# Kernel optimization log

Hardware: AMD Instinct MI355X
Metric: run time of the kernel (lower is better)

Reference implementation:

```python
import jax, jax.numpy as jnp
import numpy as np

# Dimensions (match init_kwargs / input_specs)
N, F, E = 50000, 256, 200000   # nodes, in-features, edges
H, C = 4, 128                  # heads, per-head channels (hidden_dim)
G, NC = 256, 10                # graphs in batch, num_classes
EPS = 1e-16                    # PyG softmax denominator epsilon


def _lin(key, fin, fout):
    kw, kb = jax.random.split(key)
    W = jax.random.normal(kw, (fin, fout), jnp.float32) / np.float32(np.sqrt(fin))
    b = jax.random.normal(kb, (fout,), jnp.float32) * 0.01
    return W, b


def setup_inputs() -> dict:
    key = jax.random.key(0)
    ks = jax.random.split(key, 16)
    x = jax.random.normal(ks[0], (N, F), jnp.float32)
    edge_index = jax.random.randint(ks[1], (2, E), 0, N)
    batch = jnp.sort(jax.random.randint(ks[2], (N,), 0, G))
    d = {"x": x, "edge_index": edge_index, "batch": batch}
    # layer1: in=F, out=H*C (concat=True); layer2: in=H*C, out=C (concat=False, skip -> C)
    d["Wq1"], d["bq1"] = _lin(ks[3], F, H * C)
    d["Wk1"], d["bk1"] = _lin(ks[4], F, H * C)
    d["Wv1"], d["bv1"] = _lin(ks[5], F, H * C)
    d["Ws1"], d["bs1"] = _lin(ks[6], F, H * C)
    d["Wq2"], d["bq2"] = _lin(ks[7], H * C, H * C)
    d["Wk2"], d["bk2"] = _lin(ks[8], H * C, H * C)
    d["Wv2"], d["bv2"] = _lin(ks[9], H * C, H * C)
    d["Ws2"], d["bs2"] = _lin(ks[10], H * C, C)
    d["Wfc"], d["bfc"] = _lin(ks[11], C, NC)
    return d


def _tconv(x, src, dst, Wq, bq, Wk, bk, Wv, bv, Ws, bs, concat):
    """PyG TransformerConv (root_weight=True, beta=False), eval mode (no dropout)."""
    n = x.shape[0]
    q = (x @ Wq + bq).reshape(n, H, C)
    k = (x @ Wk + bk).reshape(n, H, C)
    v = (x @ Wv + bv).reshape(n, H, C)
    # per-edge scores: query from dst node i, key/value from src node j
    alpha = jnp.einsum('ehc,ehc->eh', q[dst], k[src]) / jnp.float32(np.sqrt(C))  # [E,H]
    m = jax.ops.segment_max(alpha, dst, num_segments=n)          # [N,H]
    e = jnp.exp(alpha - m[dst])                                  # [E,H]
    s = jax.ops.segment_sum(e, dst, num_segments=n)              # [N,H]
    a = e / (s[dst] + EPS)                                       # segment softmax over dst
    msg = jax.ops.segment_sum(a[:, :, None] * v[src], dst, num_segments=n)  # [N,H,C]
    out = msg.reshape(n, H * C) if concat else msg.mean(axis=1)
    return out + x @ Ws + bs  # root/skip connection


def reference(x, edge_index, batch,
              Wq1, bq1, Wk1, bk1, Wv1, bv1, Ws1, bs1,
              Wq2, bq2, Wk2, bk2, Wv2, bv2, Ws2, bs2,
              Wfc, bfc):
    src, dst = edge_index[0], edge_index[1]
    h = jax.nn.elu(_tconv(x, src, dst, Wq1, bq1, Wk1, bk1, Wv1, bv1, Ws1, bs1, True))
    # dropout is identity in eval mode
    h = jax.nn.elu(_tconv(h, src, dst, Wq2, bq2, Wk2, bk2, Wv2, bv2, Ws2, bs2, False))
    cnt = jax.ops.segment_sum(jnp.ones((h.shape[0],), h.dtype), batch, num_segments=G)
    pooled = jax.ops.segment_sum(h, batch, num_segments=G) / jnp.maximum(cnt, 1.0)[:, None]
    return jax.nn.log_softmax(pooled @ Wfc + bfc, axis=1)  # [G, NC]
```

## Files before the change

kernel.cpp:

```cpp
#include <hip/hip_runtime.h>
#include <math.h>
#include <stdint.h>

#define N_NODES 50000
#define FEAT    256
#define EDGES   200000
#define HEADS   4
#define CH      128
#define HID     512
#define NGRAPH  256
#define NCLS    10

typedef unsigned short ushort_t;
typedef unsigned int uint_t;
typedef __attribute__((ext_vector_type(8))) short bf16x8;
typedef __attribute__((ext_vector_type(4))) float f32x4;
typedef __attribute__((ext_vector_type(2))) float f32x2;

__device__ __forceinline__ ushort_t f2bf(float f) {
  uint_t u = __float_as_uint(f);
  u += 0x7FFF + ((u >> 16) & 1);
  return (ushort_t)(u >> 16);
}
__device__ __forceinline__ float bf2f(ushort_t h) {
  return __uint_as_float(((uint_t)h) << 16);
}
__device__ __forceinline__ float elu1(float x) {
  return x > 0.f ? x : __expf(x) - 1.f;
}
__device__ __forceinline__ float fastrcp(float x) {
  return __builtin_amdgcn_rcpf(x);
}
__device__ __forceinline__ void unpack8(uint4 w, float* f) {
  f[0] = bf2f((ushort_t)w.x); f[1] = bf2f((ushort_t)(w.x >> 16));
  f[2] = bf2f((ushort_t)w.y); f[3] = bf2f((ushort_t)(w.y >> 16));
  f[4] = bf2f((ushort_t)w.z); f[5] = bf2f((ushort_t)(w.z >> 16));
  f[6] = bf2f((ushort_t)w.w); f[7] = bf2f((ushort_t)(w.w >> 16));
}
__device__ __forceinline__ void unpack8_fp8(uint2 w, float* f) {
  f32x2 a = __builtin_amdgcn_cvt_pk_f32_fp8((int)w.x, false);
  f32x2 b = __builtin_amdgcn_cvt_pk_f32_fp8((int)w.x, true);
  f32x2 c = __builtin_amdgcn_cvt_pk_f32_fp8((int)w.y, false);
  f32x2 d = __builtin_amdgcn_cvt_pk_f32_fp8((int)w.y, true);
  f[0] = a[0]; f[1] = a[1]; f[2] = b[0]; f[3] = b[1];
  f[4] = c[0]; f[5] = c[1]; f[6] = d[0]; f[7] = d[1];
}
__device__ __forceinline__ uint_t pack4_fp8(float f0, float f1, float f2, float f3) {
  int v = __builtin_amdgcn_cvt_pk_fp8_f32(f0, f1, 0, false);
  v = __builtin_amdgcn_cvt_pk_fp8_f32(f2, f3, v, true);
  return (uint_t)v;
}


__global__ __launch_bounds__(256) void gemm_bt(
    const ushort_t* __restrict__ A, const ushort_t* __restrict__ Bt,
    const float* __restrict__ bias, char* __restrict__ Cb,
    char* __restrict__ Cb2, int M, int K, int nct, int mode) {
  __shared__ __align__(16) ushort_t smem[24576];
  const int tid = threadIdx.x;
  const int lane = tid & 63, wave = tid >> 6;
  const int wr = wave >> 1, wc = wave & 1;

  int b = blockIdx.x;
  int per = nct << 3;
  int grp = b / per;
  int rem = b - grp * per;
  int rloc = rem & 7;
  int ct = rem >> 3;
  const int rowBase = (grp * 8 + rloc) * 128;
  const int colBase = ct * 128;
  if (rowBase >= M) return;

  const int s0 = tid, s1 = tid + 256;
  const int rl0 = s0 >> 2, cg0 = (s0 & 3) ^ ((rl0 >> 1) & 3);
  const int rl1 = s1 >> 2, cg1 = (s1 & 3) ^ ((rl1 >> 1) & 3);
  int ra0 = rowBase + rl0; ra0 = ra0 < M ? ra0 : M - 1;
  int ra1 = rowBase + rl1; ra1 = ra1 < M ? ra1 : M - 1;
  const ushort_t* pa0 = A + (size_t)ra0 * K + cg0 * 8;
  const ushort_t* pa1 = A + (size_t)ra1 * K + cg1 * 8;
  const ushort_t* pb0 = Bt + (size_t)(colBase + rl0) * K + cg0 * 8;
  const ushort_t* pb1 = Bt + (size_t)(colBase + rl1) * K + cg1 * 8;
  const int dA0 = s0 * 8, dA1 = s1 * 8;
  const int dB0 = 4096 + s0 * 8, dB1 = 4096 + s1 * 8;

#define GLL(gp, loff)  __builtin_amdgcn_global_load_lds( \
      (const __attribute__((address_space(1))) uint_t*)(gp), \
      (__attribute__((address_space(3))) uint_t*)(smem + (loff)), 16, 0, 0)

  const int nt = K >> 5;
  GLL(pa0, dA0);            GLL(pa1, dA1);
  GLL(pb0, dB0);            GLL(pb1, dB1);
  GLL(pa0 + 32, 8192 + dA0); GLL(pa1 + 32, 8192 + dA1);
  GLL(pb0 + 32, 8192 + dB0); GLL(pb1 + 32, 8192 + dB1);
  pa0 += 64; pa1 += 64; pb0 += 64; pb1 += 64;

  const int fr = lane & 15, c0 = lane >> 4;
  const int pswz = (c0 ^ ((fr >> 1) & 3)) * 8;
  const int aOff = (wr * 64 + fr) * 32 + pswz;
  const int bOff = 4096 + (wc * 64 + fr) * 32 + pswz;

  f32x4 acc[4][4] = {};
  asm volatile("s_waitcnt vmcnt(4)" ::: "memory");
  __builtin_amdgcn_s_barrier();
  __builtin_amdgcn_sched_barrier(0);

  int cur = 0, nxt = 2;
  for (int t = 0; t < nt; ++t) {
    const ushort_t* bufc = smem + cur * 8192;
    const bool pf = (t + 2) < nt;
    bf16x8 af[4], bfr[4];
    af[0] = *(const bf16x8*)(bufc + aOff);
#pragma unroll
    for (int j = 0; j < 4; ++j) bfr[j] = *(const bf16x8*)(bufc + bOff + j * 512);
#pragma unroll
    for (int i = 1; i < 4; ++i) af[i] = *(const bf16x8*)(bufc + aOff + i * 512);
    if (pf) {
      int lo = nxt * 8192;
      GLL(pa0, lo + dA0); GLL(pa1, lo + dA1);
      GLL(pb0, lo + dB0); GLL(pb1, lo + dB1);
      pa0 += 32; pa1 += 32; pb0 += 32; pb1 += 32;
    }
#pragma unroll
    for (int i = 0; i < 4; ++i)
#pragma unroll
      for (int j = 0; j < 4; ++j)
        acc[i][j] = __builtin_amdgcn_mfma_f32_16x16x32_bf16(af[i], bfr[j], acc[i][j], 0, 0, 0);
    asm volatile("s_waitcnt lgkmcnt(0)" ::: "memory");
    if (pf)                asm volatile("s_waitcnt vmcnt(4)" ::: "memory");
    else if (t + 1 < nt)   asm volatile("s_waitcnt vmcnt(0)" ::: "memory");
    __builtin_amdgcn_s_barrier();
    __builtin_amdgcn_sched_barrier(0);
    cur = cur == 2 ? 0 : cur + 1;
    nxt = nxt == 2 ? 0 : nxt + 1;
  }
#undef GLL

  char* obase; int ostride, koff, isfp8;
  if (mode == 1) {
    int H = colBase >> 9, sel = (colBase >> 7) & 3;
    if (sel == 0)      { obase = Cb;  ostride = 2304; koff = H * 256; isfp8 = 0; }
    else if (sel == 3) { obase = Cb2; ostride = 1024; koff = H * 256; isfp8 = 0; }
    else { obase = Cb; ostride = 2304;
           koff = 1024 + H * 256 + (sel == 2 ? 8 : 0); isfp8 = 1; }
  } else {
    obase = Cb; ostride = 2304;
    if (colBase == 768) { koff = 2048; isfp8 = 0; }
    else {
      int n2 = (colBase < 768) ? colBase : colBase - 896;
      int hb = (colBase < 768) ? 0 : 2;
      int hh = hb + n2 / 384, r = n2 % 384, sel = r >> 7;
      if (sel == 0) { koff = hh * 256; isfp8 = 0; }
      else          { koff = 1024 + hh * 256 + (sel == 2 ? 8 : 0); isfp8 = 1; }
    }
  }

  ushort_t* wbuf = smem + wave * 2048;
  const int rq = lane >> 4, fc = lane & 15;
  float bv[4];
#pragma unroll
  for (int j = 0; j < 4; ++j) bv[j] = bias[colBase + wc * 64 + j * 16 + fc];
#pragma unroll
  for (int h = 0; h < 2; ++h) {
#pragma unroll
    for (int ii = 0; ii < 2; ++ii) {
      int i = h * 2 + ii;
#pragma unroll
      for (int j = 0; j < 4; ++j)
#pragma unroll
        for (int r = 0; r < 4; ++r) {
          int rl = ii * 16 + rq * 4 + r;
          int cl = j * 16 + fc;
          int cs = cl ^ (rq << 4);
          wbuf[rl * 64 + cs] = f2bf(acc[i][j][r] + bv[j]);
        }
    }
    int ci = lane & 7;
    int rbase = lane >> 3;
#pragma unroll
    for (int rg = 0; rg < 4; ++rg) {
      int rr = rg * 8 + rbase;
      int rowg = rowBase + wr * 64 + h * 32 + rr;
      int cg = ci ^ (((rr >> 2) & 3) << 1);
      uint4 val = *(const uint4*)(wbuf + rr * 64 + (ci << 3));
      if (rowg < M) {
        char* dstRow = obase + (size_t)rowg * ostride + koff;
        if (!isfp8) {
          *(uint4*)(dstRow + (wc * 64 + cg * 8) * 2) = val;
        } else {
          float f[8];
          f[0] = bf2f((ushort_t)val.x); f[1] = bf2f((ushort_t)(val.x >> 16));
          f[2] = bf2f((ushort_t)val.y); f[3] = bf2f((ushort_t)(val.y >> 16));
          f[4] = bf2f((ushort_t)val.z); f[5] = bf2f((ushort_t)(val.z >> 16));
          f[6] = bf2f((ushort_t)val.w); f[7] = bf2f((ushort_t)(val.w >> 16));
          uint2 o;
          o.x = pack4_fp8(f[0], f[1], f[2], f[3]);
          o.y = pack4_fp8(f[4], f[5], f[6], f[7]);
          *(uint2*)(dstRow + ((wc * 8 + cg) << 4)) = o;
        }
      }
    }
  }
}

#define L1_W   (2048 * FEAT)
#define L2_W   (1664 * HID)
#define T1     512
#define T2     832
#define NB_CVT  12500
#define NB_TP   (T1 + T2)
#define NB_BIAS 15
#define NB_ZERO 196

__global__ __launch_bounds__(256) void prep_all(
    const float* __restrict__ x, ushort_t* __restrict__ xb,
    const float* __restrict__ Wq1, const float* __restrict__ Wk1,
    const float* __restrict__ Wv1, const float* __restrict__ Ws1,
    const float* __restrict__ Wq2, const float* __restrict__ Wk2,
    const float* __restrict__ Wv2, const float* __restrict__ Ws2,
    const float* __restrict__ bq1, const float* __restrict__ bk1,
    const float* __restrict__ bv1, const float* __restrict__ bs1,
    const float* __restrict__ bq2, const float* __restrict__ bk2,
    const float* __restrict__ bv2, const float* __restrict__ bs2,
    ushort_t* __restrict__ W1t, ushort_t* __restrict__ W2t,
    float* __restrict__ Bh1, float* __restrict__ Bh2,
    int* __restrict__ deg, int* __restrict__ counter,
    int* __restrict__ gstart, int* __restrict__ gend) {
  __shared__ float tile[32][33];
  int blk = blockIdx.x;
  if (blk < NB_CVT) {
    int i = blk * 256 + threadIdx.x;
    float4 f = *(const float4*)(x + (size_t)i * 4);
    uint_t lo = (uint_t)f2bf(f.x) | ((uint_t)f2bf(f.y) << 16);
    uint_t hi = (uint_t)f2bf(f.z) | ((uint_t)f2bf(f.w) << 16);
    ((uint2*)xb)[i] = make_uint2(lo, hi);
    return;
  }
  blk -= NB_CVT;
  if (blk < NB_TP) {
    int t = blk;
    const float* W; int ldw, c0, n0, k0, ldk; ushort_t* dst;
    if (t < T1) {
      int nb = t >> 3, kb = t & 7;
      n0 = nb * 32; k0 = kb * 32; ldk = FEAT; dst = W1t;
      int p = n0 >> 10, n1 = n0 & 1023, hh = n1 >> 9, sel = (n1 >> 7) & 3;
      c0 = (2 * p + hh) * CH + (n1 & (CH - 1));
      W = sel == 0 ? Wq1 : sel == 1 ? Wk1 : sel == 2 ? Wv1 : Ws1;
      ldw = HID;
    } else {
      t -= T1;
      int nb = t >> 4, kb = t & 15;
      n0 = nb * 32; k0 = kb * 32; ldk = HID; dst = W2t;
      if (n0 < 768 || n0 >= 896) {
        int n2 = (n0 < 768) ? n0 : n0 - 896;
        int hb = (n0 < 768) ? 0 : 2;
        int hh = hb + n2 / 384, r = n2 % 384, sel = r >> 7;
        c0 = hh * CH + (r & (CH - 1));
        W = sel == 0 ? Wq2 : sel == 1 ? Wk2 : Wv2;
        ldw = HID;
      } else {
        c0 = n0 - 768; W = Ws2; ldw = CH;
      }
    }
    int col = threadIdx.x & 31, rw = threadIdx.x >> 5;
#pragma unroll
    for (int ph = 0; ph < 4; ++ph) {
      int kk = rw + ph * 8;
      tile[kk][col] = W[(size_t)(k0 + kk) * ldw + c0 + col];
    }
    __syncthreads();
#pragma unroll
    for (int ph = 0; ph < 4; ++ph) {
      int dn = rw + ph * 8;
      dst[(size_t)(n0 + dn) * ldk + k0 + col] = f2bf(tile[col][dn]);
    }
    return;
  }
  blk -= NB_TP;
  if (blk < NB_BIAS) {
    int n = blk * 256 + threadIdx.x;
    if (n < 2048) {
      int p = n >> 10, n1 = n & 1023, hh = n1 >> 9, sel = (n1 >> 7) & 3;
      int c = (2 * p + hh) * CH + (n1 & (CH - 1));
      const float* bb = sel == 0 ? bq1 : sel == 1 ? bk1 : sel == 2 ? bv1 : bs1;
      Bh1[n] = bb[c];
    } else if (n < 2048 + 1664) {
      int n2 = n - 2048;
      if (n2 < 768 || n2 >= 896) {
        int nn = (n2 < 768) ? n2 : n2 - 896;
        int hb = (n2 < 768) ? 0 : 2;
        int hh = hb + nn / 384, r = nn % 384, sel = r >> 7;
        int c = hh * CH + (r & (CH - 1));
        const float* bb = sel == 0 ? bq2 : sel == 1 ? bk2 : bv2;
        Bh2[n2] = bb[c];
      } else {
        Bh2[n2] = bs2[n2 - 768];
      }
    }
    return;
  }
  blk -= NB_BIAS;
  {
    int i = blk * 256 + threadIdx.x;
    if (i < N_NODES) deg[i] = 0;
    if (i < NGRAPH) { gstart[i] = 0; gend[i] = 0; }
    if (i == 0) counter[0] = 0;
  }
}

__global__ void hist_bounds_kernel(const int* __restrict__ dst, int* __restrict__ deg,
                                   const int* __restrict__ batch,
                                   int* __restrict__ gstart, int* __restrict__ gend) {
  int t = blockIdx.x * blockDim.x + threadIdx.x;
  if (t < EDGES) atomicAdd(&deg[dst[t]], 1);
  if (t < N_NODES) {
    int b = batch[t];
    if (t == 0 || batch[t - 1] != b) gstart[b] = t;
    if (t == N_NODES - 1 || batch[t + 1] != b) gend[b] = t + 1;
  }
}

__global__ void alloc_kernel(const int* __restrict__ deg, int* __restrict__ counter,
                             int* __restrict__ start, int* __restrict__ cursor) {
  int i = blockIdx.x * blockDim.x + threadIdx.x;
  int lane = threadIdx.x & 63;
  int v = (i < N_NODES) ? deg[i] : 0;
  int sum = v;
#pragma unroll
  for (int off = 1; off < 64; off <<= 1) {
    int t = __shfl_up(sum, off);
    if (lane >= off) sum += t;
  }
  int excl = sum - v;
  int waveTot = __shfl(sum, 63);
  int base = 0;
  if (lane == 63) base = atomicAdd(counter, waveTot);
  base = __shfl(base, 63);
  if (i < N_NODES) {
    start[i] = base + excl;
    cursor[i] = base + excl;
  }
}

__global__ void scatter_kernel(const int* __restrict__ src, const int* __restrict__ dst,
                               int* __restrict__ cursor, int* __restrict__ csr) {
  int e = blockIdx.x * blockDim.x + threadIdx.x;
  if (e < EDGES) {
    int pos = atomicAdd(&cursor[dst[e]], 1);
    csr[pos] = src[e];
  }
}

#define INV_SQRT_CH 0.08838834764831845f

__global__ __launch_bounds__(256) void attn1_kernel(
    const char* __restrict__ BIG, const int* __restrict__ start,
    const int* __restrict__ deg, const int* __restrict__ csr,
    ushort_t* __restrict__ H1b) {
  int wave = threadIdx.x >> 6, lane = threadIdx.x & 63;
  int li = lane & 15, g = lane >> 4;
  int i = blockIdx.x * 4 + wave;
  if (i >= N_NODES) return;
  int beg = start[i], end = beg + deg[i];
  const char* ip = BIG + (size_t)i * 2304;
  float q[4][8];
#pragma unroll
  for (int h = 0; h < 4; ++h)
    unpack8(*(const uint4*)(ip + h * 256 + li * 16), q[h]);
  float s[4] = {}, a[4][8] = {};
  for (int e0 = beg; e0 < end; e0 += 4) {
    int eg = e0 + g;
    bool valid = eg < end;
    int j = csr[valid ? eg : beg];
    const char* jp = BIG + (size_t)j * 2304 + 1024;
    uint4 kv[4];
#pragma unroll
    for (int h = 0; h < 4; ++h) kv[h] = *(const uint4*)(jp + h * 256 + li * 16);
#pragma unroll
    for (int h = 0; h < 4; ++h) {
      float kf[8];
      unpack8_fp8(make_uint2(kv[h].x, kv[h].y), kf);
      float pd = q[h][0]*kf[0]+q[h][1]*kf[1]+q[h][2]*kf[2]+q[h][3]*kf[3]+
                 q[h][4]*kf[4]+q[h][5]*kf[5]+q[h][6]*kf[6]+q[h][7]*kf[7];
#pragma unroll
      for (int ox = 1; ox <= 8; ox <<= 1) pd += __shfl_xor(pd, ox);
      float w = valid ? __expf(pd * INV_SQRT_CH) : 0.f;
      float vf[8];
      unpack8_fp8(make_uint2(kv[h].z, kv[h].w), vf);
      s[h] += w;
#pragma unroll
      for (int c = 0; c < 8; ++c) a[h][c] = fmaf(w, vf[c], a[h][c]);
    }
  }
#pragma unroll
  for (int ox = 16; ox <= 32; ox <<= 1) {
#pragma unroll
    for (int h = 0; h < 4; ++h) {
      s[h] += __shfl_xor(s[h], ox);
#pragma unroll
      for (int c = 0; c < 8; ++c) a[h][c] += __shfl_xor(a[h][c], ox);
    }
  }
  if (g != 0) return;
  ushort_t* orow = H1b + (size_t)i * HID + li * 8;
#pragma unroll
  for (int h = 0; h < 4; ++h) {
    float inv = fastrcp(s[h] + 1e-16f);
    float sk[8];
    unpack8(*(const uint4*)(orow + h * CH), sk);
    uint4 ow;
    uint_t* op = (uint_t*)&ow;
#pragma unroll
    for (int c = 0; c < 4; ++c) {
      float o0 = elu1(a[h][2 * c] * inv + sk[2 * c]);
      float o1 = elu1(a[h][2 * c + 1] * inv + sk[2 * c + 1]);
      op[c] = (uint_t)f2bf(o0) | ((uint_t)f2bf(o1) << 16);
    }
    *(uint4*)(orow + h * CH) = ow;
  }
}

__global__ __launch_bounds__(256) void attn2_kernel(
    const char* __restrict__ BIG, const int* __restrict__ start,
    const int* __restrict__ deg, const int* __restrict__ csr,
    ushort_t* __restrict__ POut) {
  int wave = threadIdx.x >> 6, lane = threadIdx.x & 63;
  int li = lane & 15, g = lane >> 4;
  int i = blockIdx.x * 4 + wave;
  if (i >= N_NODES) return;
  int beg = start[i], end = beg + deg[i];
  const char* ip = BIG + (size_t)i * 2304;
  float q[4][8];
#pragma unroll
  for (int h = 0; h < 4; ++h)
    unpack8(*(const uint4*)(ip + h * 256 + li * 16), q[h]);
  float s[4] = {}, a[4][8] = {};
  for (int e0 = beg; e0 < end; e0 += 4) {
    int eg = e0 + g;
    bool valid = eg < end;
    int j = csr[valid ? eg : beg];
    const char* jp = BIG + (size_t)j * 2304 + 1024;
    uint4 kv[4];
#pragma unroll
    for (int h = 0; h < 4; ++h) kv[h] = *(const uint4*)(jp + h * 256 + li * 16);
#pragma unroll
    for (int h = 0; h < 4; ++h) {
      float kf[8];
      unpack8_fp8(make_uint2(kv[h].x, kv[h].y), kf);
      float pd = q[h][0]*kf[0]+q[h][1]*kf[1]+q[h][2]*kf[2]+q[h][3]*kf[3]+
                 q[h][4]*kf[4]+q[h][5]*kf[5]+q[h][6]*kf[6]+q[h][7]*kf[7];
#pragma unroll
      for (int ox = 1; ox <= 8; ox <<= 1) pd += __shfl_xor(pd, ox);
      float w = valid ? __expf(pd * INV_SQRT_CH) : 0.f;
      float vf[8];
      unpack8_fp8(make_uint2(kv[h].z, kv[h].w), vf);
      s[h] += w;
#pragma unroll
      for (int c = 0; c < 8; ++c) a[h][c] = fmaf(w, vf[c], a[h][c]);
    }
  }
#pragma unroll
  for (int ox = 16; ox <= 32; ox <<= 1) {
#pragma unroll
    for (int h = 0; h < 4; ++h) {
      s[h] += __shfl_xor(s[h], ox);
#pragma unroll
      for (int c = 0; c < 8; ++c) a[h][c] += __shfl_xor(a[h][c], ox);
    }
  }
  if (g != 0) return;
  float o[8] = {};
#pragma unroll
  for (int h = 0; h < 4; ++h) {
    float inv = 0.25f * fastrcp(s[h] + 1e-16f);
#pragma unroll
    for (int c = 0; c < 8; ++c) o[c] = fmaf(a[h][c], inv, o[c]);
  }
  uint4 ow;
  uint_t* op = (uint_t*)&ow;
#pragma unroll
  for (int c = 0; c < 4; ++c)
    op[c] = (uint_t)f2bf(o[2 * c]) | ((uint_t)f2bf(o[2 * c + 1]) << 16);
  *(uint4*)(POut + (size_t)i * CH + li * 8) = ow;
}

__global__ __launch_bounds__(256) void pool_cls(
    const ushort_t* __restrict__ POut, const char* __restrict__ BIG,
    const int* __restrict__ gstart, const int* __restrict__ gend,
    const float* __restrict__ Wfc, const float* __restrict__ bfc,
    float* __restrict__ out) {
  int g = blockIdx.x;
  int t = threadIdx.x;
  int c = t & (CH - 1), rr = t >> 7;
  int s0 = gstart[g], e0 = gend[g];
  float sum = 0.f;
  for (int i = s0 + rr; i < e0; i += 2) {
    float sk = bf2f(*(const ushort_t*)(BIG + (size_t)i * 2304 + 2048 + c * 2));
    float m0 = bf2f(POut[(size_t)i * CH + c]);
    sum += elu1(sk + m0);
  }
  __shared__ float sh[256];
  __shared__ float p[CH];
  __shared__ float red[CH];
  __shared__ float logits[NCLS];
  sh[t] = sum;
  __syncthreads();
  if (t < CH) {
    float cnt = fmaxf((float)(e0 - s0), 1.f);
    p[t] = (sh[t] + sh[t + CH]) / cnt;
  }
  for (int cc = 0; cc < NCLS; ++cc) {
    __syncthreads();
    if (t < CH) red[t] = p[t] * Wfc[t * NCLS + cc];
    __syncthreads();
    for (int off = 64; off > 0; off >>= 1) {
      if (t < off) red[t] += red[t + off];
      __syncthreads();
    }
    if (t == 0) logits[cc] = red[0] + bfc[cc];
  }
  __syncthreads();
  if (t == 0) {
    float mx = -INFINITY;
    for (int cc = 0; cc < NCLS; ++cc) mx = fmaxf(mx, logits[cc]);
    float se = 0.f;
    for (int cc = 0; cc < NCLS; ++cc) se += expf(logits[cc] - mx);
    float ls = mx + logf(se);
    for (int cc = 0; cc < NCLS; ++cc) out[g * NCLS + cc] = logits[cc] - ls;
  }
}

extern "C" void kernel_launch(void* const* d_in, const int* in_sizes, int n_in,
                              void* d_out, int out_size, void* d_ws, size_t ws_size,
                              hipStream_t stream) {
  const float* x    = (const float*)d_in[0];
  const int*   ei   = (const int*)d_in[1];
  const int*   batch= (const int*)d_in[2];
  const float* Wq1 = (const float*)d_in[3];  const float* bq1 = (const float*)d_in[4];
  const float* Wk1 = (const float*)d_in[5];  const float* bk1 = (const float*)d_in[6];
  const float* Wv1 = (const float*)d_in[7];  const float* bv1 = (const float*)d_in[8];
  const float* Ws1 = (const float*)d_in[9];  const float* bs1 = (const float*)d_in[10];
  const float* Wq2 = (const float*)d_in[11]; const float* bq2 = (const float*)d_in[12];
  const float* Wk2 = (const float*)d_in[13]; const float* bk2 = (const float*)d_in[14];
  const float* Wv2 = (const float*)d_in[15]; const float* bv2 = (const float*)d_in[16];
  const float* Ws2 = (const float*)d_in[17]; const float* bs2 = (const float*)d_in[18];
  const float* Wfc = (const float*)d_in[19]; const float* bfc = (const float*)d_in[20];
  float* out = (float*)d_out;

  ushort_t* xb     = (ushort_t*)d_ws;
  ushort_t* POut   = (ushort_t*)d_ws;
  char*     BIG    = (char*)(xb + (size_t)N_NODES * FEAT);
  ushort_t* H1b    = (ushort_t*)(BIG + (size_t)N_NODES * 2304);
  ushort_t* W1t    = H1b + (size_t)N_NODES * HID;
  float*    Bh1    = (float*)(W1t + L1_W);
  ushort_t* W2t    = (ushort_t*)(Bh1 + 2048);
  float*    Bh2    = (float*)(W2t + L2_W);
  int* deg    = (int*)(Bh2 + 1664);
  int* start  = deg + N_NODES;
  int* cursor = start + N_NODES;
  int* csr    = cursor + N_NODES;
  int* gstart = csr + EDGES;
  int* gend   = gstart + NGRAPH;
  int* counter= gend + NGRAPH;

  const int* srcp = ei;
  const int* dstp = ei + EDGES;

  prep_all<<<NB_CVT + NB_TP + NB_BIAS + NB_ZERO, 256, 0, stream>>>(
      x, xb, Wq1, Wk1, Wv1, Ws1, Wq2, Wk2, Wv2, Ws2,
      bq1, bk1, bv1, bs1, bq2, bk2, bv2, bs2,
      W1t, W2t, Bh1, Bh2, deg, counter, gstart, gend);
  hist_bounds_kernel<<<(EDGES + 255) / 256, 256, 0, stream>>>(dstp, deg, batch, gstart, gend);
  alloc_kernel<<<(N_NODES + 255) / 256, 256, 0, stream>>>(deg, counter, start, cursor);
  scatter_kernel<<<(EDGES + 255) / 256, 256, 0, stream>>>(srcp, dstp, cursor, csr);

  const int ga = (N_NODES + 3) / 4;

  gemm_bt<<<49 * 8 * 16, 256, 0, stream>>>(
      xb, W1t, Bh1, BIG, (char*)H1b, N_NODES, FEAT, 16, 1);
  attn1_kernel<<<ga, 256, 0, stream>>>(BIG, start, deg, csr, H1b);

  gemm_bt<<<49 * 8 * 13, 256, 0, stream>>>(
      H1b, W2t, Bh2, BIG, (char*)H1b, N_NODES, HID, 13, 2);
  attn2_kernel<<<ga, 256, 0, stream>>>(BIG, start, deg, csr, POut);

  pool_cls<<<NGRAPH, 256, 0, stream>>>(POut, BIG, gstart, gend, Wfc, bfc, out);
}
```

Baseline: 520.7 us.

## Map each 16-lane group to one head and prefetch next neighbor's K/V

Rewrites both attention kernels so that each 16-lane group of a wave owns one head and walks all edges, instead of each group taking every fourth edge across all four heads. This removes the cross-group shuffle reduction of s and a in layer 1, and in layer 2 reduces only the head-mean output. It cuts register use per thread from 4x8 accumulators to 8. A software prefetch loads the next neighbor's K/V row while the current edge is computed. The trade-off is a serial per-edge loop with a dependent index load, giving less memory-level parallelism per wave on high-degree nodes.

```diff
diff --git a/kernel.cpp b/kernel.cpp
--- a/kernel.cpp
+++ b/kernel.cpp
@@ -361,62 +361,47 @@
   int i = blockIdx.x * 4 + wave;
   if (i >= N_NODES) return;
   int beg = start[i], end = beg + deg[i];
-  const char* ip = BIG + (size_t)i * 2304;
-  float q[4][8];
-#pragma unroll
-  for (int h = 0; h < 4; ++h)
-    unpack8(*(const uint4*)(ip + h * 256 + li * 16), q[h]);
-  float s[4] = {}, a[4][8] = {};
-  for (int e0 = beg; e0 < end; e0 += 4) {
-    int eg = e0 + g;
-    bool valid = eg < end;
-    int j = csr[valid ? eg : beg];
-    const char* jp = BIG + (size_t)j * 2304 + 1024;
-    uint4 kv[4];
-#pragma unroll
-    for (int h = 0; h < 4; ++h) kv[h] = *(const uint4*)(jp + h * 256 + li * 16);
-#pragma unroll
-    for (int h = 0; h < 4; ++h) {
+  const int kvoff = 1024 + g * 256 + li * 16;
+  float q[8];
+  unpack8(*(const uint4*)(BIG + (size_t)i * 2304 + g * 256 + li * 16), q);
+  float s = 0.f, a[8] = {};
+  if (beg < end) {
+    int j = csr[beg];
+    uint4 kv = *(const uint4*)(BIG + (size_t)j * 2304 + kvoff);
+    for (int e = beg; e < end; ++e) {
+      int en = e + 1 < end ? e + 1 : e;
+      int jn = csr[en];
+      uint4 kvn = *(const uint4*)(BIG + (size_t)jn * 2304 + kvoff);
       float kf[8];
-      unpack8_fp8(make_uint2(kv[h].x, kv[h].y), kf);
-      float pd = q[h][0]*kf[0]+q[h][1]*kf[1]+q[h][2]*kf[2]+q[h][3]*kf[3]+
-                 q[h][4]*kf[4]+q[h][5]*kf[5]+q[h][6]*kf[6]+q[h][7]*kf[7];
-#pragma unroll
-      for (int ox = 1; ox <= 8; ox <<= 1) pd += __shfl_xor(pd, ox);
-      float w = valid ? __expf(pd * INV_SQRT_CH) : 0.f;
+      unpack8_fp8(make_uint2(kv.x, kv.y), kf);
+      float pd = q[0]*kf[0]+q[1]*kf[1]+q[2]*kf[2]+q[3]*kf[3]+
+                 q[4]*kf[4]+q[5]*kf[5]+q[6]*kf[6]+q[7]*kf[7];
+      pd += __shfl_xor(pd, 1);
+      pd += __shfl_xor(pd, 2);
+      pd += __shfl_xor(pd, 4);
+      pd += __shfl_xor(pd, 8);
+      float w = __expf(pd * INV_SQRT_CH);
       float vf[8];
-      unpack8_fp8(make_uint2(kv[h].z, kv[h].w), vf);
-      s[h] += w;
-#pragma unroll
-      for (int c = 0; c < 8; ++c) a[h][c] = fmaf(w, vf[c], a[h][c]);
-    }
-  }
-#pragma unroll
-  for (int ox = 16; ox <= 32; ox <<= 1) {
-#pragma unroll
-    for (int h = 0; h < 4; ++h) {
-      s[h] += __shfl_xor(s[h], ox);
-#pragma unroll
-      for (int c = 0; c < 8; ++c) a[h][c] += __shfl_xor(a[h][c], ox);
-    }
-  }
-  if (g != 0) return;
-  ushort_t* orow = H1b + (size_t)i * HID + li * 8;
-#pragma unroll
-  for (int h = 0; h < 4; ++h) {
-    float inv = fastrcp(s[h] + 1e-16f);
-    float sk[8];
-    unpack8(*(const uint4*)(orow + h * CH), sk);
-    uint4 ow;
-    uint_t* op = (uint_t*)&ow;
-#pragma unroll
-    for (int c = 0; c < 4; ++c) {
-      float o0 = elu1(a[h][2 * c] * inv + sk[2 * c]);
-      float o1 = elu1(a[h][2 * c + 1] * inv + sk[2 * c + 1]);
-      op[c] = (uint_t)f2bf(o0) | ((uint_t)f2bf(o1) << 16);
-    }
-    *(uint4*)(orow + h * CH) = ow;
-  }
+      unpack8_fp8(make_uint2(kv.z, kv.w), vf);
+      s += w;
+#pragma unroll
+      for (int c = 0; c < 8; ++c) a[c] = fmaf(w, vf[c], a[c]);
+      kv = kvn;
+    }
+  }
+  float inv = fastrcp(s + 1e-16f);
+  ushort_t* op8 = H1b + (size_t)i * HID + g * CH + li * 8;
+  float sk[8];
+  unpack8(*(const uint4*)op8, sk);
+  uint4 ow;
+  uint_t* op = (uint_t*)&ow;
+#pragma unroll
+  for (int c = 0; c < 4; ++c) {
+    float o0 = elu1(a[2 * c] * inv + sk[2 * c]);
+    float o1 = elu1(a[2 * c + 1] * inv + sk[2 * c + 1]);
+    op[c] = (uint_t)f2bf(o0) | ((uint_t)f2bf(o1) << 16);
+  }
+  *(uint4*)op8 = ow;
 }
 
 __global__ __launch_bounds__(256) void attn2_kernel(
@@ -428,53 +413,43 @@
   int i = blockIdx.x * 4 + wave;
   if (i >= N_NODES) return;
   int beg = start[i], end = beg + deg[i];
-  const char* ip = BIG + (size_t)i * 2304;
-  float q[4][8];
-#pragma unroll
-  for (int h = 0; h < 4; ++h)
-    unpack8(*(const uint4*)(ip + h * 256 + li * 16), q[h]);
-  float s[4] = {}, a[4][8] = {};
-  for (int e0 = beg; e0 < end; e0 += 4) {
-    int eg = e0 + g;
-    bool valid = eg < end;
-    int j = csr[valid ? eg : beg];
-    const char* jp = BIG + (size_t)j * 2304 + 1024;
-    uint4 kv[4];
-#pragma unroll
-    for (int h = 0; h < 4; ++h) kv[h] = *(const uint4*)(jp + h * 256 + li * 16);
-#pragma unroll
-    for (int h = 0; h < 4; ++h) {
+  const int kvoff = 1024 + g * 256 + li * 16;
+  float q[8];
+  unpack8(*(const uint4*)(BIG + (size_t)i * 2304 + g * 256 + li * 16), q);
+  float s = 0.f, a[8] = {};
+  if (beg < end) {
+    int j = csr[beg];
+    uint4 kv = *(const uint4*)(BIG + (size_t)j * 2304 + kvoff);
+    for (int e = beg; e < end; ++e) {
+      int en = e + 1 < end ? e + 1 : e;
+      int jn = csr[en];
+      uint4 kvn = *(const uint4*)(BIG + (size_t)jn * 2304 + kvoff);
       float kf[8];
-      unpack8_fp8(make_uint2(kv[h].x, kv[h].y), kf);
-      float pd = q[h][0]*kf[0]+q[h][1]*kf[1]+q[h][2]*kf[2]+q[h][3]*kf[3]+
-                 q[h][4]*kf[4]+q[h][5]*kf[5]+q[h][6]*kf[6]+q[h][7]*kf[7];
-#pragma unroll
-      for (int ox = 1; ox <= 8; ox <<= 1) pd += __shfl_xor(pd, ox);
-      float w = valid ? __expf(pd * INV_SQRT_CH) : 0.f;
+      unpack8_fp8(make_uint2(kv.x, kv.y), kf);
+      float pd = q[0]*kf[0]+q[1]*kf[1]+q[2]*kf[2]+q[3]*kf[3]+
+                 q[4]*kf[4]+q[5]*kf[5]+q[6]*kf[6]+q[7]*kf[7];
+      pd += __shfl_xor(pd, 1);
+      pd += __shfl_xor(pd, 2);
+      pd += __shfl_xor(pd, 4);
+      pd += __shfl_xor(pd, 8);
+      float w = __expf(pd * INV_SQRT_CH);
       float vf[8];
-      unpack8_fp8(make_uint2(kv[h].z, kv[h].w), vf);
-      s[h] += w;
-#pragma unroll
-      for (int c = 0; c < 8; ++c) a[h][c] = fmaf(w, vf[c], a[h][c]);
-    }
-  }
-#pragma unroll
-  for (int ox = 16; ox <= 32; ox <<= 1) {
-#pragma unroll
-    for (int h = 0; h < 4; ++h) {
-      s[h] += __shfl_xor(s[h], ox);
-#pragma unroll
-      for (int c = 0; c < 8; ++c) a[h][c] += __shfl_xor(a[h][c], ox);
-    }
-  }
+      unpack8_fp8(make_uint2(kv.z, kv.w), vf);
+      s += w;
+#pragma unroll
+      for (int c = 0; c < 8; ++c) a[c] = fmaf(w, vf[c], a[c]);
+      kv = kvn;
+    }
+  }
+  float inv = 0.25f * fastrcp(s + 1e-16f);
+  float o[8];
+#pragma unroll
+  for (int c = 0; c < 8; ++c) o[c] = a[c] * inv;
+#pragma unroll
+  for (int ox = 16; ox <= 32; ox <<= 1)
+#pragma unroll
+    for (int c = 0; c < 8; ++c) o[c] += __shfl_xor(o[c], ox);
   if (g != 0) return;
-  float o[8] = {};
-#pragma unroll
-  for (int h = 0; h < 4; ++h) {
-    float inv = 0.25f * fastrcp(s[h] + 1e-16f);
-#pragma unroll
-    for (int c = 0; c < 8; ++c) o[c] = fmaf(a[h][c], inv, o[c]);
-  }
   uint4 ow;
   uint_t* op = (uint_t*)&ow;
 #pragma unroll
```

Result: faster. 472.6 us (-9.2%).
